# Kernel optimization log

Hardware: AMD Instinct MI355X
Metric: run time of the kernel (lower is better)

## Reference

```python
import jax, jax.numpy as jnp
import numpy as np

MARGIN = 1.0
EPS = 1e-6
DIAG_BIG = 99999.0


def setup_inputs() -> dict:
    key = jax.random.key(0)
    x = jax.random.normal(key, (16384, 256), dtype=jnp.float32)
    # HardNet descriptors are unit-L2 normalized (the distance formula assumes it)
    x = x / jnp.linalg.norm(x, axis=1, keepdims=True)
    return {"x": x}


def reference(x) -> jnp.ndarray:
    cnt = x.shape[0] // 2
    a = x[:cnt]          # [N, d] anchors
    p = x[cnt:]          # [N, d] positives
    # pairwise unit-L2 distance: sqrt((1 - a.p^T + eps) * 2)
    dmat = jnp.sqrt((1.0 - jnp.matmul(a, p.T) + EPS) * 2.0)  # [N, N]
    pos = jnp.diagonal(dmat)                                  # [N]
    # mask diagonal with large constant, then row/col mins = hard negatives
    masked = dmat + jnp.eye(cnt, dtype=dmat.dtype) * DIAG_BIG
    min_a = jnp.min(masked, axis=0)   # best negative anchor per positive
    min_p = jnp.min(masked, axis=1)   # best negative positive per anchor
    neg = jnp.minimum(min_a, min_p)   # [N]
    return jnp.mean(jnp.clip(MARGIN - neg + pos, 0.0))
```

## Files before the change

### kernel.cpp

```cpp
#include <hip/hip_runtime.h>
#include <hip/hip_fp8.h>


#define CNT    8192
#define KDIM   256
#define BIGF   3.0e38f
#define SCALE1 0x7F7F7F7F

typedef float f32x4  __attribute__((ext_vector_type(4)));
typedef float f32x16 __attribute__((ext_vector_type(16)));
typedef int   v8i    __attribute__((ext_vector_type(8)));

union frag8 { uint4 q[2]; v8i v; };

__device__ __forceinline__ unsigned short f2bf(float f) {
    unsigned u = __float_as_uint(f);
    u += 0x7FFFu + ((u >> 16) & 1u);
    return (unsigned short)(u >> 16);
}

__device__ __forceinline__ unsigned cvt4_fp8(float a, float b, float c, float d) {
#if __has_builtin(__builtin_amdgcn_cvt_pk_fp8_f32)
    unsigned v = __builtin_amdgcn_cvt_pk_fp8_f32(a, b, 0, false);
    v = __builtin_amdgcn_cvt_pk_fp8_f32(c, d, v, true);
    return v;
#else
    return (unsigned)__hip_fp8_e4m3(a).__x |
           ((unsigned)__hip_fp8_e4m3(b).__x << 8) |
           ((unsigned)__hip_fp8_e4m3(c).__x << 16) |
           ((unsigned)__hip_fp8_e4m3(d).__x << 24);
#endif
}


__global__ __launch_bounds__(256) void convert_mx_kernel(
    const float* __restrict__ x, unsigned char* __restrict__ xb,
    unsigned* __restrict__ mins)
{
    int T    = blockIdx.x * 256 + threadIdx.x;
    int lane = T & 63;
    int h    = (T >> 6) & 1;
    int c    = T >> 7;
    int kc64 = c & 3;
    int rg   = c >> 2;
    int row  = rg * 32 + (lane & 31);
    int col0 = kc64 * 64 + (lane >> 5) * 32 + h * 16;
    const float* src = x + (size_t)row * KDIM + col0;
    float4 u0 = *(const float4*)(src);
    float4 u1 = *(const float4*)(src + 4);
    float4 u2 = *(const float4*)(src + 8);
    float4 u3 = *(const float4*)(src + 12);
    uint4 w;
    w.x = cvt4_fp8(u0.x, u0.y, u0.z, u0.w);
    w.y = cvt4_fp8(u1.x, u1.y, u1.z, u1.w);
    w.z = cvt4_fp8(u2.x, u2.y, u2.z, u2.w);
    w.w = cvt4_fp8(u3.x, u3.y, u3.z, u3.w);
    *(uint4*)(xb + (size_t)T * 16) = w;
    if (T < 2 * CNT) mins[T] = 0x7F7FFFFFu;
}

#define TST 136
__global__ __launch_bounds__(256, 2) void dist9_kernel(
    const unsigned char* __restrict__ Ab, const unsigned char* __restrict__ Pb,
    unsigned* __restrict__ g_rowmin, unsigned* __restrict__ g_colmin,
    float* __restrict__ g_pos)
{
    __shared__ float T[64 * TST];

    const int tid  = threadIdx.x;
    const int l    = blockIdx.x;
    const int xcd  = l & 7;
    const int i    = l >> 3;
    const int bm   = (xcd >> 1) * 16 + (i & 15);
    const int bn   = (xcd & 1) * 16 + (i >> 4);

    const int wave = tid >> 6;
    const int lane = tid & 63;
    const int l31  = lane & 31;
    const int kh   = lane >> 5;
    const int wm   = wave >> 1;
    const int wn   = wave & 1;

    f32x16 acc[2][4];
    #pragma unroll
    for (int a = 0; a < 2; a++)
        #pragma unroll
        for (int b = 0; b < 4; b++)
            #pragma unroll
            for (int r = 0; r < 16; r++)
                acc[a][b][r] = 0.f;

    const char* Abase = (const char*)Ab + lane * 16;
    const char* Pbase = (const char*)Pb + lane * 16;
    size_t a_off[2], b_off[4];
    #pragma unroll
    for (int mi = 0; mi < 2; mi++)
        a_off[mi] = (size_t)(bm * 4 + wm * 2 + mi) << 13;
    #pragma unroll
    for (int ni = 0; ni < 4; ni++)
        b_off[ni] = (size_t)(bn * 8 + wn * 4 + ni) << 13;

    frag8 ca[2], cb[4], na[2], nb[4];
    #pragma unroll
    for (int mi = 0; mi < 2; mi++) {
        ca[mi].q[0] = *(const uint4*)(Abase + a_off[mi]);
        ca[mi].q[1] = *(const uint4*)(Abase + a_off[mi] + 1024);
    }
    #pragma unroll
    for (int ni = 0; ni < 4; ni++) {
        cb[ni].q[0] = *(const uint4*)(Pbase + b_off[ni]);
        cb[ni].q[1] = *(const uint4*)(Pbase + b_off[ni] + 1024);
    }
    #pragma unroll
    for (int kc = 0; kc < 4; kc++) {
        if (kc < 3) {
            #pragma unroll
            for (int mi = 0; mi < 2; mi++) {
                na[mi].q[0] = *(const uint4*)(Abase + a_off[mi] + (kc + 1) * 2048);
                na[mi].q[1] = *(const uint4*)(Abase + a_off[mi] + (kc + 1) * 2048 + 1024);
            }
            #pragma unroll
            for (int ni = 0; ni < 4; ni++) {
                nb[ni].q[0] = *(const uint4*)(Pbase + b_off[ni] + (kc + 1) * 2048);
                nb[ni].q[1] = *(const uint4*)(Pbase + b_off[ni] + (kc + 1) * 2048 + 1024);
            }
        }
        #pragma unroll
        for (int mi = 0; mi < 2; mi++)
            #pragma unroll
            for (int ni = 0; ni < 4; ni++)
                acc[mi][ni] = __builtin_amdgcn_mfma_scale_f32_32x32x64_f8f6f4(
                    ca[mi].v, cb[ni].v, acc[mi][ni],
                    0, 0,
                    0, SCALE1,
                    0, SCALE1);
        if (kc < 3) {
            #pragma unroll
            for (int mi = 0; mi < 2; mi++) ca[mi] = na[mi];
            #pragma unroll
            for (int ni = 0; ni < 4; ni++) cb[ni] = nb[ni];
        }
    }


    if ((bm >> 1) == bn) {
        const int dstart = (bm & 1) * 128;
        #pragma unroll
        for (int mi = 0; mi < 2; mi++)
            #pragma unroll
            for (int ni = 0; ni < 4; ni++)
                #pragma unroll
                for (int reg = 0; reg < 16; reg++) {
                    int rl = wm * 64 + mi * 32 + (reg & 3) + 8 * (reg >> 2) + 4 * kh;
                    int cl = wn * 128 + ni * 32 + l31;
                    if (cl == rl + dstart) {
                        g_pos[bm * 128 + rl] = (1.0f - acc[mi][ni][reg] + 1e-6f) * 2.0f;
                        acc[mi][ni][reg] = -BIGF;
                    }
                }
    }

    #pragma unroll
    for (int ni = 0; ni < 4; ni++) {
        float v = -BIGF;
        #pragma unroll
        for (int mi = 0; mi < 2; mi++)
            #pragma unroll
            for (int reg = 0; reg < 16; reg++)
                v = fmaxf(v, acc[mi][ni][reg]);
        v = fmaxf(v, __shfl_xor(v, 32, 64));
        if (kh == 0) {
            float tt = fmaxf((1.0f - v + 1e-6f) * 2.0f, 0.0f);
            atomicMin(&g_colmin[bn * 256 + wn * 128 + ni * 32 + l31],
                      __float_as_uint(tt));
        }
    }

    const int entry = wn * 32 + l31;
    #pragma unroll
    for (int mi = 0; mi < 2; mi++)
        #pragma unroll
        for (int q = 0; q < 4; q++) {
            f32x4 v;
            #pragma unroll
            for (int rr = 0; rr < 4; rr++) {
                float m = acc[mi][0][q * 4 + rr];
                #pragma unroll
                for (int ni = 1; ni < 4; ni++)
                    m = fmaxf(m, acc[mi][ni][q * 4 + rr]);
                v[rr] = m;
            }
            *(f32x4*)&T[entry * TST + wm * 64 + mi * 32 + q * 8 + kh * 4] = v;
        }
    __syncthreads();

    if (tid < 128) {
        int row = tid;
        float v0 = T[row], v1 = T[TST + row];
        #pragma unroll
        for (int e = 2; e < 64; e += 2) {
            v0 = fmaxf(v0, T[e * TST + row]);
            v1 = fmaxf(v1, T[(e + 1) * TST + row]);
        }
        float v = fmaxf(v0, v1);
        float tt = fmaxf((1.0f - v + 1e-6f) * 2.0f, 0.0f);
        atomicMin(&g_rowmin[bm * 128 + row], __float_as_uint(tt));
    }
}

__global__ __launch_bounds__(1024) void finalize_t_kernel(
    const unsigned* __restrict__ rm, const unsigned* __restrict__ cm,
    const float* __restrict__ post, float* __restrict__ out)
{
    float local = 0.f;
    for (int i = threadIdx.x; i < CNT; i += 1024) {
        float t   = fminf(__uint_as_float(rm[i]), __uint_as_float(cm[i]));
        float neg = sqrtf(fmaxf(t, 0.f));
        float pos = sqrtf(fmaxf(post[i], 0.f));
        local += fmaxf(1.0f - neg + pos, 0.0f);
    }
    #pragma unroll
    for (int m = 1; m < 64; m <<= 1) local += __shfl_xor(local, m, 64);
    __shared__ float wsum[16];
    if ((threadIdx.x & 63) == 0) wsum[threadIdx.x >> 6] = local;
    __syncthreads();
    if (threadIdx.x == 0) {
        float s = 0.f;
        #pragma unroll
        for (int w = 0; w < 16; w++) s += wsum[w];
        out[0] = s * (1.0f / (float)CNT);
    }
}


#define BM 128
#define BN 128
#define BK 64
#define KST (BK + 8)

typedef __bf16 bf16x8 __attribute__((ext_vector_type(8)));

__global__ __launch_bounds__(256) void init_min_kernel(unsigned* buf, int n) {
    int i = blockIdx.x * 256 + threadIdx.x;
    if (i < n) buf[i] = 0x7F7FFFFFu;
}

__global__ __launch_bounds__(256) void dist_tile_kernel(
    const float* __restrict__ A, const float* __restrict__ P,
    unsigned* __restrict__ g_rowmin, unsigned* __restrict__ g_colmin,
    float* __restrict__ g_pos)
{
    __shared__ unsigned short As[BM * KST];
    __shared__ unsigned short Bs[BN * KST];
    __shared__ unsigned redrow[BM];
    __shared__ unsigned redcol[BN];

    const int tid  = threadIdx.x;
    const int bm   = blockIdx.y;
    const int bn   = blockIdx.x;
    const int wave = tid >> 6;
    const int lane = tid & 63;
    const int quad = lane >> 4;
    const int l15  = lane & 15;
    const int m_off = (wave >> 1) * 64;
    const int n_off = (wave & 1) * 64;

    if (tid < BM) redrow[tid] = 0x7F7FFFFFu;
    if (tid < BN) redcol[tid] = 0x7F7FFFFFu;

    f32x4 acc[4][4];
    #pragma unroll
    for (int i = 0; i < 4; i++)
        #pragma unroll
        for (int j = 0; j < 4; j++)
            acc[i][j] = (f32x4){0.f, 0.f, 0.f, 0.f};

    const int srow = tid >> 4;
    const int scol = tid & 15;

    for (int kc = 0; kc < KDIM / BK; kc++) {
        #pragma unroll
        for (int i = 0; i < 8; i++) {
            int r = srow + i * 16;
            float4 va = *(const float4*)(A + (size_t)(bm * BM + r) * KDIM + kc * BK + scol * 4);
            float4 vb = *(const float4*)(P + (size_t)(bn * BN + r) * KDIM + kc * BK + scol * 4);
            ushort4 wa, wb;
            wa.x = f2bf(va.x); wa.y = f2bf(va.y); wa.z = f2bf(va.z); wa.w = f2bf(va.w);
            wb.x = f2bf(vb.x); wb.y = f2bf(vb.y); wb.z = f2bf(vb.z); wb.w = f2bf(vb.w);
            *(ushort4*)(&As[r * KST + scol * 4]) = wa;
            *(ushort4*)(&Bs[r * KST + scol * 4]) = wb;
        }
        __syncthreads();
        #pragma unroll
        for (int ks = 0; ks < BK / 32; ks++) {
            bf16x8 af[4], bfr[4];
            #pragma unroll
            for (int mi = 0; mi < 4; mi++)
                af[mi] = *(const bf16x8*)(&As[(m_off + mi * 16 + l15) * KST + ks * 32 + quad * 8]);
            #pragma unroll
            for (int ni = 0; ni < 4; ni++)
                bfr[ni] = *(const bf16x8*)(&Bs[(n_off + ni * 16 + l15) * KST + ks * 32 + quad * 8]);
            #pragma unroll
            for (int mi = 0; mi < 4; mi++)
                #pragma unroll
                for (int ni = 0; ni < 4; ni++)
                    acc[mi][ni] = __builtin_amdgcn_mfma_f32_16x16x32_bf16(
                        af[mi], bfr[ni], acc[mi][ni], 0, 0, 0);
        }
        __syncthreads();
    }

    float rmin[4][4], cmin[4];
    #pragma unroll
    for (int mi = 0; mi < 4; mi++)
        #pragma unroll
        for (int r = 0; r < 4; r++) rmin[mi][r] = BIGF;
    #pragma unroll
    for (int ni = 0; ni < 4; ni++) cmin[ni] = BIGF;

    const int grow0 = bm * BM + m_off + quad * 4;
    const int gcol0 = bn * BN + n_off + l15;

    #pragma unroll
    for (int mi = 0; mi < 4; mi++)
        #pragma unroll
        for (int ni = 0; ni < 4; ni++) {
            int gcol = gcol0 + ni * 16;
            #pragma unroll
            for (int r = 0; r < 4; r++) {
                int grow = grow0 + mi * 16 + r;
                float s = acc[mi][ni][r];
                float d = sqrtf((1.0f - s + 1e-6f) * 2.0f);
                float dm = d;
                if (grow == gcol) { g_pos[grow] = d; dm = BIGF; }
                rmin[mi][r] = fminf(rmin[mi][r], dm);
                cmin[ni]    = fminf(cmin[ni], dm);
            }
        }

    #pragma unroll
    for (int mi = 0; mi < 4; mi++)
        #pragma unroll
        for (int r = 0; r < 4; r++) {
            float v = rmin[mi][r];
            v = fminf(v, __shfl_xor(v, 1, 64));
            v = fminf(v, __shfl_xor(v, 2, 64));
            v = fminf(v, __shfl_xor(v, 4, 64));
            v = fminf(v, __shfl_xor(v, 8, 64));
            rmin[mi][r] = v;
        }
    #pragma unroll
    for (int ni = 0; ni < 4; ni++) {
        float v = cmin[ni];
        v = fminf(v, __shfl_xor(v, 16, 64));
        v = fminf(v, __shfl_xor(v, 32, 64));
        cmin[ni] = v;
    }

    if (l15 == 0) {
        #pragma unroll
        for (int mi = 0; mi < 4; mi++)
            #pragma unroll
            for (int r = 0; r < 4; r++)
                atomicMin(&redrow[m_off + mi * 16 + quad * 4 + r],
                          __float_as_uint(rmin[mi][r]));
    }
    if (quad == 0) {
        #pragma unroll
        for (int ni = 0; ni < 4; ni++)
            atomicMin(&redcol[n_off + ni * 16 + l15], __float_as_uint(cmin[ni]));
    }
    __syncthreads();

    if (tid < 128) atomicMin(&g_rowmin[bm * BM + tid], redrow[tid]);
    else           atomicMin(&g_colmin[bn * BN + (tid - 128)], redcol[tid - 128]);
}

__global__ __launch_bounds__(1024) void finalize_kernel(
    const unsigned* __restrict__ g_rowmin, const unsigned* __restrict__ g_colmin,
    const float* __restrict__ g_pos, float* __restrict__ out)
{
    float local = 0.f;
    for (int i = threadIdx.x; i < CNT; i += 1024) {
        float neg = fminf(__uint_as_float(g_rowmin[i]), __uint_as_float(g_colmin[i]));
        float v = 1.0f - neg + g_pos[i];
        local += fmaxf(v, 0.0f);
    }
    #pragma unroll
    for (int m = 1; m < 64; m <<= 1) local += __shfl_xor(local, m, 64);
    __shared__ float wsum[16];
    if ((threadIdx.x & 63) == 0) wsum[threadIdx.x >> 6] = local;
    __syncthreads();
    if (threadIdx.x == 0) {
        float s = 0.f;
        #pragma unroll
        for (int w = 0; w < 16; w++) s += wsum[w];
        out[0] = s * (1.0f / (float)CNT);
    }
}


extern "C" void kernel_launch(void* const* d_in, const int* in_sizes, int n_in,
                              void* d_out, int out_size, void* d_ws, size_t ws_size,
                              hipStream_t stream) {
    const float* x = (const float*)d_in[0];
    float* out = (float*)d_out;

    const size_t fp8_bytes = (size_t)2 * CNT * KDIM;
    const size_t need = fp8_bytes + (size_t)2 * CNT * 4 + (size_t)CNT * 4;

    if (ws_size >= need) {
        unsigned char* xb   = (unsigned char*)d_ws;
        unsigned*      mins = (unsigned*)((char*)d_ws + fp8_bytes);
        float*         pos  = (float*)(mins + 2 * CNT);
        convert_mx_kernel<<<dim3(1024), dim3(256), 0, stream>>>(x, xb, mins);
        dist9_kernel<<<dim3(2048), dim3(256), 0, stream>>>(
            xb, xb + (size_t)CNT * KDIM, mins, mins + CNT, pos);
        finalize_t_kernel<<<dim3(1), dim3(1024), 0, stream>>>(mins, mins + CNT, pos, out);
    } else {
        unsigned* rowmin = (unsigned*)d_ws;
        unsigned* colmin = rowmin + CNT;
        float*    pos    = (float*)(colmin + CNT);
        init_min_kernel<<<dim3(2 * CNT / 256), dim3(256), 0, stream>>>(rowmin, 2 * CNT);
        dist_tile_kernel<<<dim3(CNT / BN, CNT / BM), dim3(256), 0, stream>>>(
            x, x + (size_t)CNT * KDIM, rowmin, colmin, pos);
        finalize_kernel<<<dim3(1), dim3(1024), 0, stream>>>(rowmin, colmin, pos, out);
    }
}
```

Before: 92.41 us.

## Stage fp8 operand tiles through double-buffered LDS with direct global-to-LDS loads

Replaces the per-wave direct global register loads of A/B fragments with cooperative global_load_lds staging into a double-buffered shared-memory tile, so each block loads every K-chunk once and waves read fragments from LDS. Each wave previously loaded its own fragments, so B rows were fetched redundantly across waves; sharing them cuts global/L2 traffic. It also raises wave priority around the MFMA burst. The cost is extra barriers and vmcnt waits per K-chunk and a larger LDS footprint (48KB), which may limit occupancy at two blocks per CU.

```diff
diff --git a/kernel.cpp b/kernel.cpp
--- a/kernel.cpp
+++ b/kernel.cpp
@@ -59,13 +59,39 @@
     if (T < 2 * CNT) mins[T] = 0x7F7FFFFFu;
 }
 
-#define TST 136
-__global__ __launch_bounds__(256, 2) void dist9_kernel(
-    const unsigned char* __restrict__ Ab, const unsigned char* __restrict__ Pb,
+__device__ __forceinline__ void stage_kc(
+    const char* __restrict__ Ab, const char* __restrict__ Pb,
+    char* lbuf, int bm, int bn, int kc, int wave, int lane)
+{
+    #pragma unroll
+    for (int t = 0; t < 6; t++) {
+        const int o  = wave * 6 + t;
+        const int cc = o >> 1;
+        const int h  = o & 1;
+        const char* src;
+        if (cc < 4)
+            src = Ab + (((bm * 4 + cc) << 13) + kc * 2048);
+        else
+            src = Pb + (((bn * 8 + (cc - 4)) << 13) + kc * 2048);
+        src += h * 1024 + lane * 16;
+        __builtin_amdgcn_global_load_lds(
+            (const __attribute__((address_space(1))) void*)src,
+            (__attribute__((address_space(3))) void*)(lbuf + cc * 2048 + h * 1024),
+            16, 0, 0);
+    }
+}
+
+#define TST  136
+#define LBUF 24576
+__global__ __launch_bounds__(256, 2) void dist11_kernel(
+    const unsigned char* __restrict__ Ab_, const unsigned char* __restrict__ Pb_,
     unsigned* __restrict__ g_rowmin, unsigned* __restrict__ g_colmin,
     float* __restrict__ g_pos)
 {
-    __shared__ float T[64 * TST];
+    __shared__ char smem[2 * LBUF];
+
+    const char* Ab = (const char*)Ab_;
+    const char* Pb = (const char*)Pb_;
 
     const int tid  = threadIdx.x;
     const int l    = blockIdx.x;
@@ -90,55 +116,46 @@
             for (int r = 0; r < 16; r++)
                 acc[a][b][r] = 0.f;
 
-    const char* Abase = (const char*)Ab + lane * 16;
-    const char* Pbase = (const char*)Pb + lane * 16;
-    size_t a_off[2], b_off[4];
-    #pragma unroll
-    for (int mi = 0; mi < 2; mi++)
-        a_off[mi] = (size_t)(bm * 4 + wm * 2 + mi) << 13;
-    #pragma unroll
-    for (int ni = 0; ni < 4; ni++)
-        b_off[ni] = (size_t)(bn * 8 + wn * 4 + ni) << 13;
-
-    frag8 ca[2], cb[4], na[2], nb[4];
-    #pragma unroll
-    for (int mi = 0; mi < 2; mi++) {
-        ca[mi].q[0] = *(const uint4*)(Abase + a_off[mi]);
-        ca[mi].q[1] = *(const uint4*)(Abase + a_off[mi] + 1024);
-    }
-    #pragma unroll
-    for (int ni = 0; ni < 4; ni++) {
-        cb[ni].q[0] = *(const uint4*)(Pbase + b_off[ni]);
-        cb[ni].q[1] = *(const uint4*)(Pbase + b_off[ni] + 1024);
-    }
+    stage_kc(Ab, Pb, smem, bm, bn, 0, wave, lane);
+    asm volatile("s_waitcnt vmcnt(0)" ::: "memory");
+    __builtin_amdgcn_s_barrier();
+
     #pragma unroll
     for (int kc = 0; kc < 4; kc++) {
-        if (kc < 3) {
-            #pragma unroll
-            for (int mi = 0; mi < 2; mi++) {
-                na[mi].q[0] = *(const uint4*)(Abase + a_off[mi] + (kc + 1) * 2048);
-                na[mi].q[1] = *(const uint4*)(Abase + a_off[mi] + (kc + 1) * 2048 + 1024);
-            }
-            #pragma unroll
-            for (int ni = 0; ni < 4; ni++) {
-                nb[ni].q[0] = *(const uint4*)(Pbase + b_off[ni] + (kc + 1) * 2048);
-                nb[ni].q[1] = *(const uint4*)(Pbase + b_off[ni] + (kc + 1) * 2048 + 1024);
-            }
-        }
+        char* cbuf = smem + (kc & 1) * LBUF;
+        char* nbuf = smem + ((kc & 1) ^ 1) * LBUF;
+        if (kc < 3)
+            stage_kc(Ab, Pb, nbuf, bm, bn, kc + 1, wave, lane);
+
+        frag8 fa[2], fb[4];
+        #pragma unroll
+        for (int mi = 0; mi < 2; mi++) {
+            const char* p = cbuf + (wm * 2 + mi) * 2048 + lane * 16;
+            fa[mi].q[0] = *(const uint4*)(p);
+            fa[mi].q[1] = *(const uint4*)(p + 1024);
+        }
+        #pragma unroll
+        for (int ni = 0; ni < 4; ni++) {
+            const char* p = cbuf + (4 + wn * 4 + ni) * 2048 + lane * 16;
+            fb[ni].q[0] = *(const uint4*)(p);
+            fb[ni].q[1] = *(const uint4*)(p + 1024);
+        }
+
+        __builtin_amdgcn_s_setprio(1);
         #pragma unroll
         for (int mi = 0; mi < 2; mi++)
             #pragma unroll
             for (int ni = 0; ni < 4; ni++)
                 acc[mi][ni] = __builtin_amdgcn_mfma_scale_f32_32x32x64_f8f6f4(
-                    ca[mi].v, cb[ni].v, acc[mi][ni],
+                    fa[mi].v, fb[ni].v, acc[mi][ni],
                     0, 0,
                     0, SCALE1,
                     0, SCALE1);
+        __builtin_amdgcn_s_setprio(0);
+
         if (kc < 3) {
-            #pragma unroll
-            for (int mi = 0; mi < 2; mi++) ca[mi] = na[mi];
-            #pragma unroll
-            for (int ni = 0; ni < 4; ni++) cb[ni] = nb[ni];
+            asm volatile("s_waitcnt vmcnt(0) lgkmcnt(0)" ::: "memory");
+            __builtin_amdgcn_s_barrier();
         }
     }
 
@@ -176,6 +193,8 @@
         }
     }
 
+    __syncthreads();
+    float* T = (float*)smem;
     const int entry = wn * 32 + l31;
     #pragma unroll
     for (int mi = 0; mi < 2; mi++)
@@ -414,7 +433,7 @@
         unsigned*      mins = (unsigned*)((char*)d_ws + fp8_bytes);
         float*         pos  = (float*)(mins + 2 * CNT);
         convert_mx_kernel<<<dim3(1024), dim3(256), 0, stream>>>(x, xb, mins);
-        dist9_kernel<<<dim3(2048), dim3(256), 0, stream>>>(
+        dist11_kernel<<<dim3(2048), dim3(256), 0, stream>>>(
             xb, xb + (size_t)CNT * KDIM, mins, mins + CNT, pos);
         finalize_t_kernel<<<dim3(1), dim3(1024), 0, stream>>>(mins, mins + CNT, pos, out);
     } else {
```

Result: slower. 95.85 us (+3.7%).
